# Kernel optimization log

Hardware: AMD Instinct MI355X
Metric: run time of the kernel (lower is better)

## Reference

```python
import jax, jax.numpy as jnp
import numpy as np

PATCH = 14      # patch_size
IMG = 896       # image H = W; feature grid = IMG // PATCH = 64
NH = 8          # first NH detections per image are persons (category_id == 1)


def _roi_mean_pool(features, boxes):
    """features [B,h,w,C]; boxes [B,D,4] cxcywh normalized. Returns [B,D,C].
    Mirrors: bbox -> pixel corners -> //patch ints -> mean over feat[y1:y2, x1:x2]."""
    B, h, w, C = features.shape
    cx, cy, bw, bh = boxes[..., 0], boxes[..., 1], boxes[..., 2], boxes[..., 3]
    x1 = jnp.floor((cx - bw / 2) * IMG / PATCH).astype(jnp.int32)  # [B,D]
    y1 = jnp.floor((cy - bh / 2) * IMG / PATCH).astype(jnp.int32)
    x2 = jnp.floor((cx + bw / 2) * IMG / PATCH).astype(jnp.int32)
    y2 = jnp.floor((cy + bh / 2) * IMG / PATCH).astype(jnp.int32)
    rgrid = jnp.arange(h)[None, None, :]
    cgrid = jnp.arange(w)[None, None, :]
    rows = ((rgrid >= y1[..., None]) & (rgrid < y2[..., None])).astype(features.dtype)  # [B,D,h]
    cols = ((cgrid >= x1[..., None]) & (cgrid < x2[..., None])).astype(features.dtype)  # [B,D,w]
    s = jnp.einsum('bdh,bhwc,bdw->bdc', rows, features, cols)
    area = rows.sum(-1) * cols.sum(-1)  # [B,D], guaranteed >= 1 by construction
    return s / area[..., None]


def setup_inputs() -> dict:
    key = jax.random.key(0)
    ks = jax.random.split(key, 12)
    B, D, C = 16, 32, 768
    features = jax.random.normal(ks[0], (B, 64, 64, C), dtype=jnp.float32)
    # valid, in-range, non-degenerate boxes (cxcywh normalized)
    cxy = jax.random.uniform(ks[1], (B, D, 2), minval=0.25, maxval=0.75)
    bwh = jax.random.uniform(ks[2], (B, D, 2), minval=0.08, maxval=0.30)
    boxes = jnp.concatenate([cxy, bwh], axis=-1).astype(jnp.float32)
    scores = jax.random.uniform(ks[3], (B, D), dtype=jnp.float32)
    # first NH detections are persons, rest are objects
    obj = jax.random.randint(ks[4], (B, D - NH), 2, 80, dtype=jnp.int32)
    labels = jnp.concatenate([jnp.ones((B, NH), jnp.int32), obj], axis=1)
    def lin(k, fin, fout):
        return (jax.random.normal(k, (fin, fout), jnp.float32) / np.sqrt(fin)).astype(jnp.float32)
    return {
        'features': features, 'boxes': boxes, 'scores': scores,
        'w1': lin(ks[5], 2 * C, 512), 'b1': jnp.zeros((512,), jnp.float32),
        'w2': lin(ks[6], 512, 256),  'b2': jnp.zeros((256,), jnp.float32),
        'w3': lin(ks[7], 256, 117),  'b3': jnp.zeros((117,), jnp.float32),
        'labels': labels,
    }


def reference(features, boxes, scores, w1, b1, w2, b2, w3, b3, labels):
    pooled = _roi_mean_pool(features, boxes)          # [B,D,C]
    hfeat, ofeat = pooled[:, :NH], pooled[:, NH:]     # persons / objects
    hs, osr = scores[:, :NH], scores[:, NH:]
    # sort each group by descending score (as in the original)
    hidx = jnp.argsort(-hs, axis=1)
    oidx = jnp.argsort(-osr, axis=1)
    hfeat = jnp.take_along_axis(hfeat, hidx[..., None], axis=1)
    ofeat = jnp.take_along_axis(ofeat, oidx[..., None], axis=1)
    B, nh, C = hfeat.shape
    no = ofeat.shape[1]
    hh = jnp.broadcast_to(hfeat[:, :, None, :], (B, nh, no, C))
    oo = jnp.broadcast_to(ofeat[:, None, :, :], (B, nh, no, C))
    pairs = jnp.concatenate([hh, oo], axis=-1).reshape(B, nh * no, 2 * C)
    x = jax.nn.relu(pairs @ w1 + b1)
    x = jax.nn.relu(x @ w2 + b2)
    return x @ w3 + b3                                # [B, nh*no, 117] relation scores
```

## Files before the change

### kernel.cpp

```cpp
#include <hip/hip_runtime.h>
#include <math.h>

#define B 16
#define D 32
#define NH 8
#define NO 24
#define C 768
#define H 64
#define W 64
#define H1 512
#define H2 256
#define H3 117
#define NP (NH * NO)

__device__ inline float4 f4add(float4 a, float4 b) {
  return make_float4(a.x + b.x, a.y + b.y, a.z + b.z, a.w + b.w);
}

__global__ __launch_bounds__(256) void roi_pool_k(
    const float* __restrict__ feat, const float* __restrict__ boxes,
    float* __restrict__ pooled) {
  int bd = blockIdx.x;
  int b = bd >> 5;
  const float* bx = boxes + (size_t)bd * 4;
  float cx = bx[0], cy = bx[1], bw = bx[2], bh = bx[3];
  int xa = (int)floorf(__fdiv_rn(__fmul_rn(cx - 0.5f * bw, 896.0f), 14.0f));
  int ya = (int)floorf(__fdiv_rn(__fmul_rn(cy - 0.5f * bh, 896.0f), 14.0f));
  int xb = (int)floorf(__fdiv_rn(__fmul_rn(cx + 0.5f * bw, 896.0f), 14.0f));
  int yb = (int)floorf(__fdiv_rn(__fmul_rn(cy + 0.5f * bh, 896.0f), 14.0f));
  xa = max(xa, 0); ya = max(ya, 0); xb = min(xb, W); yb = min(yb, H);

  int t = threadIdx.x;
  int wv = t >> 6;
  int lane = t & 63;
  int c0 = blockIdx.y * 256 + lane * 4;
  const float* fb = feat + (size_t)b * (H * W * C) + c0;

  float4 s0 = make_float4(0.f, 0.f, 0.f, 0.f);
  float4 s1 = s0, s2 = s0, s3 = s0;
  for (int y = ya + wv; y < yb; y += 4) {
    const float* fr = fb + (size_t)y * (W * C);
    int x = xa;
    for (; x + 3 < xb; x += 4) {
      float4 v0 = *(const float4*)(fr + (size_t)(x + 0) * C);
      float4 v1 = *(const float4*)(fr + (size_t)(x + 1) * C);
      float4 v2 = *(const float4*)(fr + (size_t)(x + 2) * C);
      float4 v3 = *(const float4*)(fr + (size_t)(x + 3) * C);
      s0 = f4add(s0, v0); s1 = f4add(s1, v1);
      s2 = f4add(s2, v2); s3 = f4add(s3, v3);
    }
    for (; x < xb; ++x)
      s0 = f4add(s0, *(const float4*)(fr + (size_t)x * C));
  }
  s0 = f4add(f4add(s0, s1), f4add(s2, s3));

  __shared__ float4 red[4][64];
  red[wv][lane] = s0;
  __syncthreads();
  if (wv == 0) {
    float4 a = f4add(f4add(red[0][lane], red[1][lane]),
                     f4add(red[2][lane], red[3][lane]));
    float area = (float)((yb - ya) * (xb - xa));
    float4 r;
    r.x = __fdiv_rn(a.x, area);
    r.y = __fdiv_rn(a.y, area);
    r.z = __fdiv_rn(a.z, area);
    r.w = __fdiv_rn(a.w, area);
    *(float4*)(pooled + (size_t)bd * C + c0) = r;
  }
}

__global__ __launch_bounds__(64) void sort_k(
    const float* __restrict__ scores, int* __restrict__ hidx,
    int* __restrict__ oidx) {
  int b = blockIdx.x;
  int d = threadIdx.x;
  if (d >= D) return;
  const float* s = scores + (size_t)b * D;
  float v = s[d];
  if (d < NH) {
    int r = 0;
    for (int j = 0; j < NH; ++j) {
      float u = s[j];
      if (u > v || (u == v && j < d)) ++r;
    }
    hidx[b * NH + r] = d;
  } else {
    int r = 0;
    for (int j = NH; j < D; ++j) {
      float u = s[j];
      if (u > v || (u == v && j < d)) ++r;
    }
    oidx[b * NO + r] = d - NH;
  }
}

__global__ __launch_bounds__(256) void transpose_k(
    const float* __restrict__ in, float* __restrict__ out, int R, int Cc) {
  __shared__ float tile[32][33];
  int c0 = blockIdx.x * 32, r0 = blockIdx.y * 32;
  int tx = threadIdx.x, ty = threadIdx.y;
  #pragma unroll
  for (int i = 0; i < 32; i += 8) {
    int r = r0 + ty + i, c = c0 + tx;
    if (r < R && c < Cc) tile[ty + i][tx] = in[(size_t)r * Cc + c];
  }
  __syncthreads();
  #pragma unroll
  for (int i = 0; i < 32; i += 8) {
    int c = c0 + ty + i, r = r0 + tx;
    if (c < Cc && r < R) out[(size_t)c * R + r] = tile[tx][ty + i];
  }
}

__global__ __launch_bounds__(128) void l1_k(
    const float* __restrict__ pooled, const float* __restrict__ w1T,
    float* __restrict__ php, float* __restrict__ pop) {
  int t = threadIdx.x;
  int tile = blockIdx.x;
  int colh = blockIdx.y;
  int kh = blockIdx.z;
  int rr0 = tile * 8;
  int b = rr0 >> 5;
  bool human = ((tile & 3) == 0);
  int kbase = kh * 384;
  size_t wk = (size_t)(human ? 0 : C) + kbase;
  int cA = colh * 256 + t;
  const float* wA = w1T + (size_t)cA * (2 * C) + wk;
  const float* wB = wA + (size_t)128 * (2 * C);
  const float* ap = pooled + (size_t)rr0 * C + kbase;

  float accA[8], accB[8];
  #pragma unroll
  for (int r = 0; r < 8; ++r) { accA[r] = 0.f; accB[r] = 0.f; }

  float4 wa = *(const float4*)wA;
  float4 wb = *(const float4*)wB;
  for (int k = 0; k < 384; k += 4) {
    float4 wa_n = *(const float4*)(wA + k + 4);
    float4 wb_n = *(const float4*)(wB + k + 4);
    #pragma unroll
    for (int r = 0; r < 8; ++r) {
      const float* ar = ap + (size_t)r * C + k;
      float a0 = ar[0], a1 = ar[1], a2 = ar[2], a3 = ar[3];
      accA[r] = fmaf(a0, wa.x, accA[r]);
      accA[r] = fmaf(a1, wa.y, accA[r]);
      accA[r] = fmaf(a2, wa.z, accA[r]);
      accA[r] = fmaf(a3, wa.w, accA[r]);
      accB[r] = fmaf(a0, wb.x, accB[r]);
      accB[r] = fmaf(a1, wb.y, accB[r]);
      accB[r] = fmaf(a2, wb.z, accB[r]);
      accB[r] = fmaf(a3, wb.w, accB[r]);
    }
    wa = wa_n; wb = wb_n;
  }

  if (human) {
    #pragma unroll
    for (int r = 0; r < 8; ++r) {
      size_t row = (size_t)kh * (B * NH) + b * NH + r;
      php[row * H1 + cA] = accA[r];
      php[row * H1 + cA + 128] = accB[r];
    }
  } else {
    int dbase = (tile & 3) * 8 - NH;
    #pragma unroll
    for (int r = 0; r < 8; ++r) {
      size_t row = (size_t)kh * (B * NO) + b * NO + dbase + r;
      pop[row * H1 + cA] = accA[r];
      pop[row * H1 + cA + 128] = accB[r];
    }
  }
}

__global__ __launch_bounds__(128) void pair_k(
    const float* __restrict__ php, const float* __restrict__ pop,
    const float* __restrict__ b1, const int* __restrict__ hidx,
    const int* __restrict__ oidx, float* __restrict__ x1) {
  int row = blockIdx.x;
  int b = row / NP;
  int p = row % NP;
  int i = p / NO, j = p % NO;
  int hi = hidx[b * NH + i];
  int oj = oidx[b * NO + j];
  int t = threadIdx.x;
  const float4* h0 = (const float4*)(php + ((size_t)(b * NH + hi)) * H1);
  const float4* h1 = (const float4*)(php + ((size_t)(B * NH + b * NH + hi)) * H1);
  const float4* o0 = (const float4*)(pop + ((size_t)(b * NO + oj)) * H1);
  const float4* o1 = (const float4*)(pop + ((size_t)(B * NO + b * NO + oj)) * H1);
  const float4* bb = (const float4*)b1;
  float4 v = f4add(f4add(h0[t], h1[t]), f4add(o0[t], o1[t]));
  v = f4add(v, bb[t]);
  v.x = fmaxf(v.x, 0.f); v.y = fmaxf(v.y, 0.f);
  v.z = fmaxf(v.z, 0.f); v.w = fmaxf(v.w, 0.f);
  ((float4*)(x1 + (size_t)row * H1))[t] = v;
}

__global__ __launch_bounds__(128) void l2_k(
    const float* __restrict__ x1, const float* __restrict__ w2T,
    const float* __restrict__ b2, float* __restrict__ x2) {
  int t = threadIdx.x;
  size_t r0 = (size_t)blockIdx.x * 8;
  const float* wA = w2T + (size_t)t * H1;
  const float* wB = w2T + (size_t)(t + 128) * H1;
  const float* ap = x1 + r0 * H1;

  float accA[8], accB[8];
  #pragma unroll
  for (int r = 0; r < 8; ++r) { accA[r] = 0.f; accB[r] = 0.f; }

  float4 wa = *(const float4*)wA;
  float4 wb = *(const float4*)wB;
  for (int k = 0; k < H1; k += 4) {
    float4 wa_n = *(const float4*)(wA + k + 4);
    float4 wb_n = *(const float4*)(wB + k + 4);
    #pragma unroll
    for (int r = 0; r < 8; ++r) {
      const float* ar = ap + (size_t)r * H1 + k;
      float a0 = ar[0], a1 = ar[1], a2 = ar[2], a3 = ar[3];
      accA[r] = fmaf(a0, wa.x, accA[r]);
      accA[r] = fmaf(a1, wa.y, accA[r]);
      accA[r] = fmaf(a2, wa.z, accA[r]);
      accA[r] = fmaf(a3, wa.w, accA[r]);
      accB[r] = fmaf(a0, wb.x, accB[r]);
      accB[r] = fmaf(a1, wb.y, accB[r]);
      accB[r] = fmaf(a2, wb.z, accB[r]);
      accB[r] = fmaf(a3, wb.w, accB[r]);
    }
    wa = wa_n; wb = wb_n;
  }

  float bA = b2[t], bB = b2[t + 128];
  #pragma unroll
  for (int r = 0; r < 8; ++r) {
    x2[(r0 + r) * H2 + t] = fmaxf(accA[r] + bA, 0.f);
    x2[(r0 + r) * H2 + t + 128] = fmaxf(accB[r] + bB, 0.f);
  }
}

__global__ __launch_bounds__(128) void l3_k(
    const float* __restrict__ x2, const float* __restrict__ w3T,
    const float* __restrict__ b3, float* __restrict__ out) {
  int t = threadIdx.x;
  if (t >= H3) return;
  size_t r0 = (size_t)blockIdx.x * 8;
  const float* wc = w3T + (size_t)t * H2;
  const float* ap = x2 + r0 * H2;

  float acc[8];
  #pragma unroll
  for (int r = 0; r < 8; ++r) acc[r] = 0.f;

  float4 wa = *(const float4*)wc;
  for (int k = 0; k < H2; k += 4) {
    float4 wa_n = *(const float4*)(wc + k + 4);
    #pragma unroll
    for (int r = 0; r < 8; ++r) {
      const float* ar = ap + (size_t)r * H2 + k;
      acc[r] = fmaf(ar[0], wa.x, acc[r]);
      acc[r] = fmaf(ar[1], wa.y, acc[r]);
      acc[r] = fmaf(ar[2], wa.z, acc[r]);
      acc[r] = fmaf(ar[3], wa.w, acc[r]);
    }
    wa = wa_n;
  }
  float bias = b3[t];
  #pragma unroll
  for (int r = 0; r < 8; ++r)
    out[(r0 + r) * H3 + t] = acc[r] + bias;
}

extern "C" void kernel_launch(void* const* d_in, const int* in_sizes, int n_in,
                              void* d_out, int out_size, void* d_ws,
                              size_t ws_size, hipStream_t stream) {
  const float* feat   = (const float*)d_in[0];
  const float* boxes  = (const float*)d_in[1];
  const float* scores = (const float*)d_in[2];
  const float* w1     = (const float*)d_in[3];
  const float* b1     = (const float*)d_in[4];
  const float* w2     = (const float*)d_in[5];
  const float* b2     = (const float*)d_in[6];
  const float* w3     = (const float*)d_in[7];
  const float* b3     = (const float*)d_in[8];
  float* out = (float*)d_out;

  float* base   = (float*)d_ws;
  float* pooled = base;
  float* w1T    = base + 393216;
  float* x2     = base;
  float* w2T    = base + 1179648;
  float* w3T    = base + 1310720;
  float* php    = base + 1340672;
  float* pop    = base + 1471744;
  float* x1     = base + 1864960;
  int*   hidx   = (int*)(base + 3437824);
  int*   oidx   = hidx + B * NH;

  roi_pool_k<<<dim3(B * D, 3), 256, 0, stream>>>(feat, boxes, pooled);
  sort_k<<<dim3(B), 64, 0, stream>>>(scores, hidx, oidx);
  transpose_k<<<dim3(16, 48), dim3(32, 8), 0, stream>>>(w1, w1T, 2 * C, H1);
  transpose_k<<<dim3(8, 16), dim3(32, 8), 0, stream>>>(w2, w2T, H1, H2);
  transpose_k<<<dim3(4, 8), dim3(32, 8), 0, stream>>>(w3, w3T, H2, H3);
  l1_k<<<dim3(64, 2, 2), 128, 0, stream>>>(pooled, w1T, php, pop);
  pair_k<<<dim3(B * NP), 128, 0, stream>>>(php, pop, b1, hidx, oidx, x1);
  l2_k<<<dim3(B * NP / 8), 128, 0, stream>>>(x1, w2T, b2, x2);
  l3_k<<<dim3(B * NP / 8), 128, 0, stream>>>(x2, w3T, b3, out);
}
```

Before: 385.3 us.

## Fuse sort, pairing and MLP layers into one kernel; drop weight transposes

Removes the three weight transpose kernels by reading w1/w2/w3 in their original row-major layout with coalesced per-thread column loads. Layer 1 now stages activations in LDS, uses a 4-way K split, and each thread computes 4 output columns. The sort, pair-sum with bias and ReLU, layer 2 and layer 3 are fused into one kernel that keeps the intermediates in shared memory, so x1/x2 no longer round-trip through global memory and fewer kernels are launched. The fused kernel recomputes the score sort in every block and has fewer, heavier blocks, which may lower occupancy.

```diff
diff --git a/kernel.cpp b/kernel.cpp
--- a/kernel.cpp
+++ b/kernel.cpp
@@ -12,6 +12,7 @@
 #define H2 256
 #define H3 117
 #define NP (NH * NO)
+#define KSPLIT 4
 
 __device__ inline float4 f4add(float4 a, float4 b) {
   return make_float4(a.x + b.x, a.y + b.y, a.z + b.z, a.w + b.w);
@@ -70,204 +71,197 @@
   }
 }
 
-__global__ __launch_bounds__(64) void sort_k(
-    const float* __restrict__ scores, int* __restrict__ hidx,
-    int* __restrict__ oidx) {
-  int b = blockIdx.x;
-  int d = threadIdx.x;
-  if (d >= D) return;
-  const float* s = scores + (size_t)b * D;
-  float v = s[d];
-  if (d < NH) {
-    int r = 0;
-    for (int j = 0; j < NH; ++j) {
-      float u = s[j];
-      if (u > v || (u == v && j < d)) ++r;
-    }
-    hidx[b * NH + r] = d;
-  } else {
-    int r = 0;
-    for (int j = NH; j < D; ++j) {
-      float u = s[j];
-      if (u > v || (u == v && j < d)) ++r;
-    }
-    oidx[b * NO + r] = d - NH;
-  }
-}
-
-__global__ __launch_bounds__(256) void transpose_k(
-    const float* __restrict__ in, float* __restrict__ out, int R, int Cc) {
-  __shared__ float tile[32][33];
-  int c0 = blockIdx.x * 32, r0 = blockIdx.y * 32;
-  int tx = threadIdx.x, ty = threadIdx.y;
-  #pragma unroll
-  for (int i = 0; i < 32; i += 8) {
-    int r = r0 + ty + i, c = c0 + tx;
-    if (r < R && c < Cc) tile[ty + i][tx] = in[(size_t)r * Cc + c];
-  }
-  __syncthreads();
-  #pragma unroll
-  for (int i = 0; i < 32; i += 8) {
-    int c = c0 + ty + i, r = r0 + tx;
-    if (c < Cc && r < R) out[(size_t)c * R + r] = tile[tx][ty + i];
-  }
-}
-
 __global__ __launch_bounds__(128) void l1_k(
-    const float* __restrict__ pooled, const float* __restrict__ w1T,
+    const float* __restrict__ pooled, const float* __restrict__ w1,
     float* __restrict__ php, float* __restrict__ pop) {
+  __shared__ float a_lds[8 * 192];
   int t = threadIdx.x;
   int tile = blockIdx.x;
-  int colh = blockIdx.y;
-  int kh = blockIdx.z;
+  int kh = blockIdx.y;
   int rr0 = tile * 8;
   int b = rr0 >> 5;
   bool human = ((tile & 3) == 0);
-  int kbase = kh * 384;
-  size_t wk = (size_t)(human ? 0 : C) + kbase;
-  int cA = colh * 256 + t;
-  const float* wA = w1T + (size_t)cA * (2 * C) + wk;
-  const float* wB = wA + (size_t)128 * (2 * C);
-  const float* ap = pooled + (size_t)rr0 * C + kbase;
-
-  float accA[8], accB[8];
+  int kbase = kh * 192;
+
+  {
+    const float* src = pooled + (size_t)rr0 * C + kbase;
+    for (int idx = t; idx < 384; idx += 128) {
+      int r = idx / 48, c = idx % 48;
+      ((float4*)a_lds)[r * 48 + c] = *(const float4*)(src + (size_t)r * C + c * 4);
+    }
+  }
+  __syncthreads();
+
+  int kg0 = (human ? 0 : C) + kbase;
+  const float* wp = w1 + (size_t)kg0 * H1 + 4 * t;
+
+  float4 acc[8];
   #pragma unroll
-  for (int r = 0; r < 8; ++r) { accA[r] = 0.f; accB[r] = 0.f; }
-
-  float4 wa = *(const float4*)wA;
-  float4 wb = *(const float4*)wB;
-  for (int k = 0; k < 384; k += 4) {
-    float4 wa_n = *(const float4*)(wA + k + 4);
-    float4 wb_n = *(const float4*)(wB + k + 4);
-    #pragma unroll
-    for (int r = 0; r < 8; ++r) {
-      const float* ar = ap + (size_t)r * C + k;
-      float a0 = ar[0], a1 = ar[1], a2 = ar[2], a3 = ar[3];
-      accA[r] = fmaf(a0, wa.x, accA[r]);
-      accA[r] = fmaf(a1, wa.y, accA[r]);
-      accA[r] = fmaf(a2, wa.z, accA[r]);
-      accA[r] = fmaf(a3, wa.w, accA[r]);
-      accB[r] = fmaf(a0, wb.x, accB[r]);
-      accB[r] = fmaf(a1, wb.y, accB[r]);
-      accB[r] = fmaf(a2, wb.z, accB[r]);
-      accB[r] = fmaf(a3, wb.w, accB[r]);
-    }
-    wa = wa_n; wb = wb_n;
+  for (int r = 0; r < 8; ++r) acc[r] = make_float4(0.f, 0.f, 0.f, 0.f);
+
+  for (int kk = 0; kk < 192; kk += 4) {
+    float4 w0 = *(const float4*)(wp + (size_t)(kk + 0) * H1);
+    float4 w1v = *(const float4*)(wp + (size_t)(kk + 1) * H1);
+    float4 w2v = *(const float4*)(wp + (size_t)(kk + 2) * H1);
+    float4 w3v = *(const float4*)(wp + (size_t)(kk + 3) * H1);
+    #pragma unroll
+    for (int r = 0; r < 8; ++r) {
+      float4 a = *(const float4*)(a_lds + r * 192 + kk);
+      acc[r].x = fmaf(a.x, w0.x, acc[r].x);
+      acc[r].y = fmaf(a.x, w0.y, acc[r].y);
+      acc[r].z = fmaf(a.x, w0.z, acc[r].z);
+      acc[r].w = fmaf(a.x, w0.w, acc[r].w);
+      acc[r].x = fmaf(a.y, w1v.x, acc[r].x);
+      acc[r].y = fmaf(a.y, w1v.y, acc[r].y);
+      acc[r].z = fmaf(a.y, w1v.z, acc[r].z);
+      acc[r].w = fmaf(a.y, w1v.w, acc[r].w);
+      acc[r].x = fmaf(a.z, w2v.x, acc[r].x);
+      acc[r].y = fmaf(a.z, w2v.y, acc[r].y);
+      acc[r].z = fmaf(a.z, w2v.z, acc[r].z);
+      acc[r].w = fmaf(a.z, w2v.w, acc[r].w);
+      acc[r].x = fmaf(a.w, w3v.x, acc[r].x);
+      acc[r].y = fmaf(a.w, w3v.y, acc[r].y);
+      acc[r].z = fmaf(a.w, w3v.z, acc[r].z);
+      acc[r].w = fmaf(a.w, w3v.w, acc[r].w);
+    }
   }
 
   if (human) {
     #pragma unroll
     for (int r = 0; r < 8; ++r) {
-      size_t row = (size_t)kh * (B * NH) + b * NH + r;
-      php[row * H1 + cA] = accA[r];
-      php[row * H1 + cA + 128] = accB[r];
+      size_t row = ((size_t)kh * B + b) * NH + r;
+      *(float4*)(php + row * H1 + 4 * t) = acc[r];
     }
   } else {
     int dbase = (tile & 3) * 8 - NH;
     #pragma unroll
     for (int r = 0; r < 8; ++r) {
-      size_t row = (size_t)kh * (B * NO) + b * NO + dbase + r;
-      pop[row * H1 + cA] = accA[r];
-      pop[row * H1 + cA + 128] = accB[r];
-    }
-  }
-}
-
-__global__ __launch_bounds__(128) void pair_k(
+      size_t row = ((size_t)kh * B + b) * NO + dbase + r;
+      *(float4*)(pop + row * H1 + 4 * t) = acc[r];
+    }
+  }
+}
+
+__global__ __launch_bounds__(128) void mlp_k(
     const float* __restrict__ php, const float* __restrict__ pop,
-    const float* __restrict__ b1, const int* __restrict__ hidx,
-    const int* __restrict__ oidx, float* __restrict__ x1) {
-  int row = blockIdx.x;
-  int b = row / NP;
-  int p = row % NP;
-  int i = p / NO, j = p % NO;
-  int hi = hidx[b * NH + i];
-  int oj = oidx[b * NO + j];
+    const float* __restrict__ scores, const float* __restrict__ b1,
+    const float* __restrict__ w2, const float* __restrict__ b2,
+    const float* __restrict__ w3, const float* __restrict__ b3,
+    float* __restrict__ out) {
+  __shared__ float x1s[8 * H1];
+  __shared__ float x2s[8 * H2];
+  __shared__ int inv[D];
   int t = threadIdx.x;
-  const float4* h0 = (const float4*)(php + ((size_t)(b * NH + hi)) * H1);
-  const float4* h1 = (const float4*)(php + ((size_t)(B * NH + b * NH + hi)) * H1);
-  const float4* o0 = (const float4*)(pop + ((size_t)(b * NO + oj)) * H1);
-  const float4* o1 = (const float4*)(pop + ((size_t)(B * NO + b * NO + oj)) * H1);
-  const float4* bb = (const float4*)b1;
-  float4 v = f4add(f4add(h0[t], h1[t]), f4add(o0[t], o1[t]));
-  v = f4add(v, bb[t]);
-  v.x = fmaxf(v.x, 0.f); v.y = fmaxf(v.y, 0.f);
-  v.z = fmaxf(v.z, 0.f); v.w = fmaxf(v.w, 0.f);
-  ((float4*)(x1 + (size_t)row * H1))[t] = v;
-}
-
-__global__ __launch_bounds__(128) void l2_k(
-    const float* __restrict__ x1, const float* __restrict__ w2T,
-    const float* __restrict__ b2, float* __restrict__ x2) {
-  int t = threadIdx.x;
-  size_t r0 = (size_t)blockIdx.x * 8;
-  const float* wA = w2T + (size_t)t * H1;
-  const float* wB = w2T + (size_t)(t + 128) * H1;
-  const float* ap = x1 + r0 * H1;
-
-  float accA[8], accB[8];
+  int blk = blockIdx.x;
+  int b = blk / 24;
+  int tile = blk % 24;
+  int i = tile / 3;
+  int j0 = (tile % 3) * 8;
+
+  if (t < D) {
+    const float* s = scores + (size_t)b * D;
+    float v = s[t];
+    if (t < NH) {
+      int r = 0;
+      for (int j = 0; j < NH; ++j) {
+        float u = s[j];
+        r += (u > v) || (u == v && j < t);
+      }
+      inv[r] = t;
+    } else {
+      int r = 0;
+      for (int j = NH; j < D; ++j) {
+        float u = s[j];
+        r += (u > v) || (u == v && j < t);
+      }
+      inv[NH + r] = t - NH;
+    }
+  }
+  __syncthreads();
+
+  int hi = inv[i];
+  float4 hs = make_float4(0.f, 0.f, 0.f, 0.f);
   #pragma unroll
-  for (int r = 0; r < 8; ++r) { accA[r] = 0.f; accB[r] = 0.f; }
-
-  float4 wa = *(const float4*)wA;
-  float4 wb = *(const float4*)wB;
-  for (int k = 0; k < H1; k += 4) {
-    float4 wa_n = *(const float4*)(wA + k + 4);
-    float4 wb_n = *(const float4*)(wB + k + 4);
-    #pragma unroll
-    for (int r = 0; r < 8; ++r) {
-      const float* ar = ap + (size_t)r * H1 + k;
-      float a0 = ar[0], a1 = ar[1], a2 = ar[2], a3 = ar[3];
-      accA[r] = fmaf(a0, wa.x, accA[r]);
-      accA[r] = fmaf(a1, wa.y, accA[r]);
-      accA[r] = fmaf(a2, wa.z, accA[r]);
-      accA[r] = fmaf(a3, wa.w, accA[r]);
-      accB[r] = fmaf(a0, wb.x, accB[r]);
-      accB[r] = fmaf(a1, wb.y, accB[r]);
-      accB[r] = fmaf(a2, wb.z, accB[r]);
-      accB[r] = fmaf(a3, wb.w, accB[r]);
-    }
-    wa = wa_n; wb = wb_n;
-  }
-
-  float bA = b2[t], bB = b2[t + 128];
+  for (int s = 0; s < KSPLIT; ++s) {
+    const float4* p = (const float4*)(php + (((size_t)s * B + b) * NH + hi) * H1);
+    hs = f4add(hs, p[t]);
+  }
+  hs = f4add(hs, ((const float4*)b1)[t]);
   #pragma unroll
   for (int r = 0; r < 8; ++r) {
-    x2[(r0 + r) * H2 + t] = fmaxf(accA[r] + bA, 0.f);
-    x2[(r0 + r) * H2 + t + 128] = fmaxf(accB[r] + bB, 0.f);
-  }
-}
-
-__global__ __launch_bounds__(128) void l3_k(
-    const float* __restrict__ x2, const float* __restrict__ w3T,
-    const float* __restrict__ b3, float* __restrict__ out) {
-  int t = threadIdx.x;
-  if (t >= H3) return;
-  size_t r0 = (size_t)blockIdx.x * 8;
-  const float* wc = w3T + (size_t)t * H2;
-  const float* ap = x2 + r0 * H2;
-
-  float acc[8];
-  #pragma unroll
-  for (int r = 0; r < 8; ++r) acc[r] = 0.f;
-
-  float4 wa = *(const float4*)wc;
-  for (int k = 0; k < H2; k += 4) {
-    float4 wa_n = *(const float4*)(wc + k + 4);
-    #pragma unroll
-    for (int r = 0; r < 8; ++r) {
-      const float* ar = ap + (size_t)r * H2 + k;
-      acc[r] = fmaf(ar[0], wa.x, acc[r]);
-      acc[r] = fmaf(ar[1], wa.y, acc[r]);
-      acc[r] = fmaf(ar[2], wa.z, acc[r]);
-      acc[r] = fmaf(ar[3], wa.w, acc[r]);
-    }
-    wa = wa_n;
-  }
-  float bias = b3[t];
-  #pragma unroll
-  for (int r = 0; r < 8; ++r)
-    out[(r0 + r) * H3 + t] = acc[r] + bias;
+    int oj = inv[NH + j0 + r];
+    float4 os = make_float4(0.f, 0.f, 0.f, 0.f);
+    #pragma unroll
+    for (int s = 0; s < KSPLIT; ++s) {
+      const float4* p = (const float4*)(pop + (((size_t)s * B + b) * NO + oj) * H1);
+      os = f4add(os, p[t]);
+    }
+    float4 x = f4add(hs, os);
+    x.x = fmaxf(x.x, 0.f); x.y = fmaxf(x.y, 0.f);
+    x.z = fmaxf(x.z, 0.f); x.w = fmaxf(x.w, 0.f);
+    *(float4*)(x1s + r * H1 + 4 * t) = x;
+  }
+  __syncthreads();
+
+  {
+    float accA[8], accB[8];
+    #pragma unroll
+    for (int r = 0; r < 8; ++r) { accA[r] = 0.f; accB[r] = 0.f; }
+    const float* wbase = w2 + 2 * t;
+    for (int kc = 0; kc < H1; kc += 4) {
+      float2 wk0 = *(const float2*)(wbase + (size_t)(kc + 0) * H2);
+      float2 wk1 = *(const float2*)(wbase + (size_t)(kc + 1) * H2);
+      float2 wk2 = *(const float2*)(wbase + (size_t)(kc + 2) * H2);
+      float2 wk3 = *(const float2*)(wbase + (size_t)(kc + 3) * H2);
+      #pragma unroll
+      for (int r = 0; r < 8; ++r) {
+        float4 a = *(const float4*)(x1s + r * H1 + kc);
+        accA[r] = fmaf(a.x, wk0.x, accA[r]);
+        accB[r] = fmaf(a.x, wk0.y, accB[r]);
+        accA[r] = fmaf(a.y, wk1.x, accA[r]);
+        accB[r] = fmaf(a.y, wk1.y, accB[r]);
+        accA[r] = fmaf(a.z, wk2.x, accA[r]);
+        accB[r] = fmaf(a.z, wk2.y, accB[r]);
+        accA[r] = fmaf(a.w, wk3.x, accA[r]);
+        accB[r] = fmaf(a.w, wk3.y, accB[r]);
+      }
+    }
+    float bA = b2[2 * t], bB = b2[2 * t + 1];
+    #pragma unroll
+    for (int r = 0; r < 8; ++r) {
+      float2 v;
+      v.x = fmaxf(accA[r] + bA, 0.f);
+      v.y = fmaxf(accB[r] + bB, 0.f);
+      *(float2*)(x2s + r * H2 + 2 * t) = v;
+    }
+  }
+  __syncthreads();
+
+  if (t < H3) {
+    float acc3[8];
+    #pragma unroll
+    for (int r = 0; r < 8; ++r) acc3[r] = 0.f;
+    const float* wbase = w3 + t;
+    for (int kc = 0; kc < H2; kc += 4) {
+      float w0 = wbase[(size_t)(kc + 0) * H3];
+      float w1v = wbase[(size_t)(kc + 1) * H3];
+      float w2v = wbase[(size_t)(kc + 2) * H3];
+      float w3v = wbase[(size_t)(kc + 3) * H3];
+      #pragma unroll
+      for (int r = 0; r < 8; ++r) {
+        float4 a = *(const float4*)(x2s + r * H2 + kc);
+        acc3[r] = fmaf(a.x, w0, acc3[r]);
+        acc3[r] = fmaf(a.y, w1v, acc3[r]);
+        acc3[r] = fmaf(a.z, w2v, acc3[r]);
+        acc3[r] = fmaf(a.w, w3v, acc3[r]);
+      }
+    }
+    float bias = b3[t];
+    size_t g0 = (size_t)b * NP + (size_t)i * NO + j0;
+    #pragma unroll
+    for (int r = 0; r < 8; ++r)
+      out[(g0 + r) * H3 + t] = acc3[r] + bias;
+  }
 }
 
 extern "C" void kernel_launch(void* const* d_in, const int* in_sizes, int n_in,
@@ -286,23 +280,11 @@
 
   float* base   = (float*)d_ws;
   float* pooled = base;
-  float* w1T    = base + 393216;
-  float* x2     = base;
-  float* w2T    = base + 1179648;
-  float* w3T    = base + 1310720;
-  float* php    = base + 1340672;
-  float* pop    = base + 1471744;
-  float* x1     = base + 1864960;
-  int*   hidx   = (int*)(base + 3437824);
-  int*   oidx   = hidx + B * NH;
+  float* php    = base + 393216;
+  float* pop    = php + 262144;
 
   roi_pool_k<<<dim3(B * D, 3), 256, 0, stream>>>(feat, boxes, pooled);
-  sort_k<<<dim3(B), 64, 0, stream>>>(scores, hidx, oidx);
-  transpose_k<<<dim3(16, 48), dim3(32, 8), 0, stream>>>(w1, w1T, 2 * C, H1);
-  transpose_k<<<dim3(8, 16), dim3(32, 8), 0, stream>>>(w2, w2T, H1, H2);
-  transpose_k<<<dim3(4, 8), dim3(32, 8), 0, stream>>>(w3, w3T, H2, H3);
-  l1_k<<<dim3(64, 2, 2), 128, 0, stream>>>(pooled, w1T, php, pop);
-  pair_k<<<dim3(B * NP), 128, 0, stream>>>(php, pop, b1, hidx, oidx, x1);
-  l2_k<<<dim3(B * NP / 8), 128, 0, stream>>>(x1, w2T, b2, x2);
-  l3_k<<<dim3(B * NP / 8), 128, 0, stream>>>(x2, w3T, b3, out);
-}
+  l1_k<<<dim3(64, KSPLIT), 128, 0, stream>>>(pooled, w1, php, pop);
+  mlp_k<<<dim3(B * 24), 128, 0, stream>>>(php, pop, scores, b1, w2, b2, w3, b3,
+                                          out);
+}
```

Result: no change. 387.7 us (+0.6%).
